# Kernel optimization log

Hardware: AMD Instinct MI355X
Metric: run time of the kernel (lower is better)

The kernel has to match this reference:

```python
import jax, jax.numpy as jnp
import numpy as np

NUM_ENTITIES = 100000
NUM_RELATIONS = 200          # 2*NUM_RELATIONS typed edges after adding inverses
DE = 200                     # entity embedding dim (= conv out channels)
DR = 200                     # relation embedding dim (in channels = DE+DR)
NUM_BASES = 4
N_NODES = 50000              # unique nodes in the extracted subgraph
N_TRIPLETS = 200000
N_EDGES = 2 * N_TRIPLETS     # forward + inverse edges


def setup_inputs() -> dict:
    key = jax.random.key(0)
    ks = jax.random.split(key, 10)
    # learned parameters
    entity_embedding = jax.random.normal(ks[0], (NUM_ENTITIES, DE), dtype=jnp.float32) * 0.05
    relation_embedding = jax.random.normal(ks[1], (NUM_RELATIONS, DR), dtype=jnp.float32) * 0.05
    # basis decomposition: W_r = sum_b att[r, b] * basis[b], basis: [B, in, out]
    xav = np.sqrt(2.0 / (DE + DR + DE)).astype(np.float32)
    basis = jax.random.normal(ks[2], (NUM_BASES, DE + DR, DE), dtype=jnp.float32) * xav
    att = jax.random.normal(ks[3], (2 * NUM_RELATIONS, NUM_BASES), dtype=jnp.float32) * 0.5
    # subgraph structure (precomputed numpy preprocessing from the torch forward)
    node_id = jax.random.randint(ks[4], (N_NODES,), 0, NUM_ENTITIES)
    src = jax.random.randint(ks[5], (N_TRIPLETS,), 0, N_NODES)
    dst = jax.random.randint(ks[6], (N_TRIPLETS,), 0, N_NODES)
    rel = jax.random.randint(ks[7], (N_TRIPLETS,), 0, NUM_RELATIONS)
    # doubling: (src->dst, rel) and inverse (dst->src, rel + NUM_RELATIONS);
    # rel_index (used to gather relation embeddings) stays un-shifted.
    edge_src = jnp.concatenate([src, dst])
    edge_dst = jnp.concatenate([dst, src])
    edge_type = jnp.concatenate([rel, rel + NUM_RELATIONS])
    rel_index = jnp.concatenate([rel, rel])
    return {
        "entity_embedding": entity_embedding,
        "relation_embedding": relation_embedding,
        "basis": basis,
        "att": att,
        "node_id": node_id,
        "edge_src": edge_src,
        "edge_dst": edge_dst,
        "edge_type": edge_type,
        "rel_index": rel_index,
        "unseen_index": 0,
    }


def reference(entity_embedding, relation_embedding, basis, att,
              node_id, edge_src, edge_dst, edge_type, rel_index, unseen_index):
    n_nodes = node_id.shape[0]
    # node features for the subgraph: [N, DE]
    x = entity_embedding[node_id]
    # per-edge relation embedding: [E, DR]
    rel = relation_embedding[rel_index]
    # message input: cat(source node emb, relation emb) -> [E, DE+DR]
    xj = jnp.concatenate([x[edge_src], rel], axis=1)
    # basis-decomposed relation-typed transform without materializing [E, in, out]:
    # project onto each basis first: [E, B, DE]
    h = jnp.einsum('ei,bio->ebo', xj, basis)
    # combine with relation-specific basis coefficients: [E, DE]
    msg = jnp.einsum('eb,ebo->eo', att[edge_type], h)
    # mean aggregation per destination node (edge_norm=None, root_weight/bias off)
    agg = jax.ops.segment_sum(msg, edge_dst, num_segments=n_nodes)
    cnt = jax.ops.segment_sum(jnp.ones(msg.shape[0], msg.dtype), edge_dst,
                              num_segments=n_nodes)
    embeddings = agg / jnp.maximum(cnt, 1.0)[:, None]
    # dropout is identity in eval mode
    return embeddings[unseen_index]
```

## Files before the change

### kernel.cpp

```cpp
#include <hip/hip_runtime.h>


#define DE 200
#define IN_DIM 400
#define ICHUNK 50
#define NCHUNK 8
#define MAXJ 32
#define FBLOCKS 256
#define TOTB (NCHUNK * MAXJ)
#define PBCAP 64
#define MAXE 128

#define WS_CNT_OFF   0
#define WS_DONE_OFF  256
#define WS_ACC_OFF   320
#define WS_LIST_OFF  1024

__global__ __launch_bounds__(256)
void filter_k(const int4* __restrict__ edge_dst4,
              const int* __restrict__ edge_dst,
              const int* __restrict__ unseen,
              int n4, int n_edges,
              int* __restrict__ ws) {
    const int b = blockIdx.x;
    const int t = threadIdx.x;
    __shared__ int s_cnt;
    __shared__ int s_list[PBCAP];
    if (t == 0) s_cnt = 0;
    __syncthreads();

    const int u = unseen[0];
    for (int idx = b * blockDim.x + t; idx < n4; idx += FBLOCKS * blockDim.x) {
        const int4 v = edge_dst4[idx];
        const int  e = idx * 4;
        if (v.x == u) { int p = atomicAdd(&s_cnt, 1); if (p < PBCAP) s_list[p] = e;     }
        if (v.y == u) { int p = atomicAdd(&s_cnt, 1); if (p < PBCAP) s_list[p] = e + 1; }
        if (v.z == u) { int p = atomicAdd(&s_cnt, 1); if (p < PBCAP) s_list[p] = e + 2; }
        if (v.w == u) { int p = atomicAdd(&s_cnt, 1); if (p < PBCAP) s_list[p] = e + 3; }
    }
    if (b == 0) {
        if (t < (n_edges & 3)) {
            const int e = n4 * 4 + t;
            if (edge_dst[e] == u) { int p = atomicAdd(&s_cnt, 1); if (p < PBCAP) s_list[p] = e; }
        }
        if (t < DE) ((float*)ws)[WS_ACC_OFF + t] = 0.f;
        if (t == DE) ws[WS_DONE_OFF] = 0;
    }
    __syncthreads();
    if (t == 0) ws[WS_CNT_OFF + b] = s_cnt;
    const int cl = s_cnt < PBCAP ? s_cnt : PBCAP;
    if (t < cl) ws[WS_LIST_OFF + b * PBCAP + t] = s_list[t];
}

__global__ __launch_bounds__(256)
void compute_k(const float* __restrict__ Eemb,
               const float* __restrict__ Remb,
               const float* __restrict__ basis,
               const float* __restrict__ att,
               const int* __restrict__ node_id,
               const int* __restrict__ edge_src,
               const int* __restrict__ edge_type,
               const int* __restrict__ rel_index,
               int* __restrict__ ws,
               float* __restrict__ out) {
    const int t = threadIdx.x;
    const int chunk = blockIdx.x;
    const int jslot = blockIdx.y;
    float* acc = (float*)ws + WS_ACC_OFF;

    __shared__ int s_counts[FBLOCKS];
    __shared__ unsigned long long s_mask[FBLOCKS / 64];
    __shared__ int s_edges[MAXE];
    __shared__ int s_total, s_listed, s_last;
    __shared__ float s_xj[ICHUNK];

    const int c = ws[WS_CNT_OFF + t];
    s_counts[t] = c;
    const unsigned long long bal = __ballot(c > 0);
    if ((t & 63) == 0) s_mask[t >> 6] = bal;
    __syncthreads();
    if (t == 0) {
        int tot = 0, listed = 0;
        for (int w = 0; w < FBLOCKS / 64; ++w) {
            unsigned long long m = s_mask[w];
            while (m) {
                const int bb = w * 64 + __builtin_ctzll(m);
                m &= m - 1;
                const int cb = s_counts[bb];
                tot += cb;
                const int cl = cb < PBCAP ? cb : PBCAP;
                for (int k = 0; k < cl && listed < MAXE; ++k)
                    s_edges[listed++] = ws[WS_LIST_OFF + bb * PBCAP + k];
            }
        }
        s_total  = tot;
        s_listed = listed;
    }
    __syncthreads();

    const int cnt  = s_listed;
    const int base = chunk * ICHUNK;

    float m = 0.f;
    bool any = false;
    for (int j = jslot; j < cnt; j += MAXJ) {
        const int e   = s_edges[j];
        const int src = edge_src[e];
        const int typ = edge_type[e];
        const int ri  = rel_index[e];
        __syncthreads();
        if (t < ICHUNK) {
            const int i = base + t;
            s_xj[t] = (i < DE) ? Eemb[(size_t)node_id[src] * DE + i]
                               : Remb[(size_t)ri * DE + (i - DE)];
        }
        __syncthreads();
        if (t < DE) {
            const float a0 = att[typ * 4 + 0];
            const float a1 = att[typ * 4 + 1];
            const float a2 = att[typ * 4 + 2];
            const float a3 = att[typ * 4 + 3];
            float h0 = 0.f, h1 = 0.f, h2 = 0.f, h3 = 0.f;
            #pragma unroll 5
            for (int ii = 0; ii < ICHUNK; ++ii) {
                const float xv  = s_xj[ii];
                const int   off = (base + ii) * DE + t;
                h0 += xv * basis[off];
                h1 += xv * basis[off + 80000];
                h2 += xv * basis[off + 160000];
                h3 += xv * basis[off + 240000];
            }
            m += a0 * h0 + a1 * h1 + a2 * h2 + a3 * h3;
            any = true;
        }
    }
    if (any) atomicAdd(&acc[t], m);

    __threadfence();
    __syncthreads();
    if (t == 0) {
        const int d = atomicAdd(&ws[WS_DONE_OFF], 1);
        s_last = (d == TOTB - 1);
    }
    __syncthreads();
    if (s_last) {
        __threadfence();
        if (t < DE) {
            const float v = atomicAdd(&acc[t], 0.f);
            int cdiv = s_total;
            if (cdiv < 1) cdiv = 1;
            out[t] = v / (float)cdiv;
        }
    }
}

extern "C" void kernel_launch(void* const* d_in, const int* in_sizes, int n_in,
                              void* d_out, int out_size, void* d_ws, size_t ws_size,
                              hipStream_t stream) {
    const float* Eemb  = (const float*)d_in[0];
    const float* Remb  = (const float*)d_in[1];
    const float* basis = (const float*)d_in[2];
    const float* att   = (const float*)d_in[3];
    const int* node_id  = (const int*)d_in[4];
    const int* edge_src = (const int*)d_in[5];
    const int* edge_dst = (const int*)d_in[6];
    const int* edge_typ = (const int*)d_in[7];
    const int* rel_idx  = (const int*)d_in[8];
    const int* unseen   = (const int*)d_in[9];
    float* out = (float*)d_out;
    int*   ws  = (int*)d_ws;

    const int n_edges = in_sizes[6];
    const int n4 = n_edges / 4;

    filter_k<<<FBLOCKS, 256, 0, stream>>>((const int4*)edge_dst, edge_dst,
                                          unseen, n4, n_edges, ws);

    dim3 cgrid(NCHUNK, MAXJ);
    compute_k<<<cgrid, 256, 0, stream>>>(Eemb, Remb, basis, att, node_id,
                                         edge_src, edge_typ, rel_idx,
                                         ws, out);
}
```

Baseline: 144.7 us.

## Reassociate per-edge basis transform into att-weighted input sums, then one GEMV per output column

The compute kernel now first forms, for each basis b, the att-weighted sum of the gathered edge inputs (a 4x400 vector), then multiplies that once by the basis matrix. Previously it ran a full per-edge projection through all bases. Each of 50 blocks prefetches its slice of basis columns into registers before the edge list is ready, and reduces through shared memory. This removes the global atomic accumulation and the last-block completion counter. In exchange, every block redundantly recomputes the 1600-entry weighted sum, and only 50 blocks run.

```diff
diff --git a/kernel.cpp b/kernel.cpp
--- a/kernel.cpp
+++ b/kernel.cpp
@@ -3,18 +3,17 @@
 
 #define DE 200
 #define IN_DIM 400
-#define ICHUNK 50
-#define NCHUNK 8
-#define MAXJ 32
+#define NB 4
+#define ROWS (NB * IN_DIM)
 #define FBLOCKS 256
-#define TOTB (NCHUNK * MAXJ)
 #define PBCAP 64
 #define MAXE 128
+#define CBLOCKS 50
+#define CPB 4
+#define KITER (ROWS / 64)
 
-#define WS_CNT_OFF   0
-#define WS_DONE_OFF  256
-#define WS_ACC_OFF   320
-#define WS_LIST_OFF  1024
+#define WS_CNT_OFF  0
+#define WS_LIST_OFF 1024
 
 __global__ __launch_bounds__(256)
 void filter_k(const int4* __restrict__ edge_dst4,
@@ -38,13 +37,9 @@
         if (v.z == u) { int p = atomicAdd(&s_cnt, 1); if (p < PBCAP) s_list[p] = e + 2; }
         if (v.w == u) { int p = atomicAdd(&s_cnt, 1); if (p < PBCAP) s_list[p] = e + 3; }
     }
-    if (b == 0) {
-        if (t < (n_edges & 3)) {
-            const int e = n4 * 4 + t;
-            if (edge_dst[e] == u) { int p = atomicAdd(&s_cnt, 1); if (p < PBCAP) s_list[p] = e; }
-        }
-        if (t < DE) ((float*)ws)[WS_ACC_OFF + t] = 0.f;
-        if (t == DE) ws[WS_DONE_OFF] = 0;
+    if (b == 0 && t < (n_edges & 3)) {
+        const int e = n4 * 4 + t;
+        if (edge_dst[e] == u) { int p = atomicAdd(&s_cnt, 1); if (p < PBCAP) s_list[p] = e; }
     }
     __syncthreads();
     if (t == 0) ws[WS_CNT_OFF + b] = s_cnt;
@@ -61,22 +56,31 @@
                const int* __restrict__ edge_src,
                const int* __restrict__ edge_type,
                const int* __restrict__ rel_index,
-               int* __restrict__ ws,
+               const int* __restrict__ ws,
                float* __restrict__ out) {
-    const int t = threadIdx.x;
-    const int chunk = blockIdx.x;
-    const int jslot = blockIdx.y;
-    float* acc = (float*)ws + WS_ACC_OFF;
+    const int t  = threadIdx.x;
+    const int c  = t & 3;
+    const int rg = t >> 2;
+    const int o  = blockIdx.x * CPB + c;
 
-    __shared__ int s_counts[FBLOCKS];
+    float rv[KITER];
+    #pragma unroll
+    for (int k = 0; k < KITER; ++k)
+        rv[k] = basis[(size_t)(rg + 64 * k) * DE + o];
+
+    __shared__ int   s_counts[FBLOCKS];
     __shared__ unsigned long long s_mask[FBLOCKS / 64];
-    __shared__ int s_edges[MAXE];
-    __shared__ int s_total, s_listed, s_last;
-    __shared__ float s_xj[ICHUNK];
+    __shared__ int   s_edges[MAXE];
+    __shared__ int   s_srcrow[MAXE];
+    __shared__ int   s_ri[MAXE];
+    __shared__ float s_att[MAXE][NB];
+    __shared__ int   s_total, s_listed;
+    __shared__ float s_y[ROWS];
+    __shared__ float s_part[256];
 
-    const int c = ws[WS_CNT_OFF + t];
-    s_counts[t] = c;
-    const unsigned long long bal = __ballot(c > 0);
+    const int cv = ws[WS_CNT_OFF + t];
+    s_counts[t] = cv;
+    const unsigned long long bal = __ballot(cv > 0);
     if ((t & 63) == 0) s_mask[t >> 6] = bal;
     __syncthreads();
     if (t == 0) {
@@ -97,60 +101,52 @@
         s_listed = listed;
     }
     __syncthreads();
+    const int cnt = s_listed;
 
-    const int cnt  = s_listed;
-    const int base = chunk * ICHUNK;
-
-    float m = 0.f;
-    bool any = false;
-    for (int j = jslot; j < cnt; j += MAXJ) {
-        const int e   = s_edges[j];
-        const int src = edge_src[e];
+    if (t < cnt) {
+        const int e = s_edges[t];
+        s_srcrow[t] = node_id[edge_src[e]];
+        s_ri[t]     = rel_index[e];
         const int typ = edge_type[e];
-        const int ri  = rel_index[e];
-        __syncthreads();
-        if (t < ICHUNK) {
-            const int i = base + t;
-            s_xj[t] = (i < DE) ? Eemb[(size_t)node_id[src] * DE + i]
-                               : Remb[(size_t)ri * DE + (i - DE)];
-        }
-        __syncthreads();
-        if (t < DE) {
-            const float a0 = att[typ * 4 + 0];
-            const float a1 = att[typ * 4 + 1];
-            const float a2 = att[typ * 4 + 2];
-            const float a3 = att[typ * 4 + 3];
-            float h0 = 0.f, h1 = 0.f, h2 = 0.f, h3 = 0.f;
-            #pragma unroll 5
-            for (int ii = 0; ii < ICHUNK; ++ii) {
-                const float xv  = s_xj[ii];
-                const int   off = (base + ii) * DE + t;
-                h0 += xv * basis[off];
-                h1 += xv * basis[off + 80000];
-                h2 += xv * basis[off + 160000];
-                h3 += xv * basis[off + 240000];
-            }
-            m += a0 * h0 + a1 * h1 + a2 * h2 + a3 * h3;
-            any = true;
-        }
-    }
-    if (any) atomicAdd(&acc[t], m);
-
-    __threadfence();
-    __syncthreads();
-    if (t == 0) {
-        const int d = atomicAdd(&ws[WS_DONE_OFF], 1);
-        s_last = (d == TOTB - 1);
+        #pragma unroll
+        for (int b = 0; b < NB; ++b) s_att[t][b] = att[typ * NB + b];
     }
     __syncthreads();
-    if (s_last) {
-        __threadfence();
-        if (t < DE) {
-            const float v = atomicAdd(&acc[t], 0.f);
-            int cdiv = s_total;
-            if (cdiv < 1) cdiv = 1;
-            out[t] = v / (float)cdiv;
+
+    for (int i = t; i < IN_DIM; i += 256) {
+        float y0 = 0.f, y1 = 0.f, y2 = 0.f, y3 = 0.f;
+        for (int j = 0; j < cnt; ++j) {
+            const float xv = (i < DE)
+                ? Eemb[(size_t)s_srcrow[j] * DE + i]
+                : Remb[(size_t)s_ri[j] * DE + (i - DE)];
+            y0 += s_att[j][0] * xv;
+            y1 += s_att[j][1] * xv;
+            y2 += s_att[j][2] * xv;
+            y3 += s_att[j][3] * xv;
         }
+        s_y[0 * IN_DIM + i] = y0;
+        s_y[1 * IN_DIM + i] = y1;
+        s_y[2 * IN_DIM + i] = y2;
+        s_y[3 * IN_DIM + i] = y3;
+    }
+    __syncthreads();
+
+    float acc = 0.f;
+    #pragma unroll
+    for (int k = 0; k < KITER; ++k)
+        acc += rv[k] * s_y[rg + 64 * k];
+
+    s_part[t] = acc;
+    __syncthreads();
+    #pragma unroll
+    for (int off = 128; off >= 4; off >>= 1) {
+        if (t < off) s_part[t] += s_part[t + off];
+        __syncthreads();
+    }
+    if (t < CPB) {
+        int cd = s_total;
+        if (cd < 1) cd = 1;
+        out[blockIdx.x * CPB + t] = s_part[t] / (float)cd;
     }
 }
 
@@ -176,8 +172,7 @@
     filter_k<<<FBLOCKS, 256, 0, stream>>>((const int4*)edge_dst, edge_dst,
                                           unseen, n4, n_edges, ws);
 
-    dim3 cgrid(NCHUNK, MAXJ);
-    compute_k<<<cgrid, 256, 0, stream>>>(Eemb, Remb, basis, att, node_id,
-                                         edge_src, edge_typ, rel_idx,
-                                         ws, out);
+    compute_k<<<CBLOCKS, 256, 0, stream>>>(Eemb, Remb, basis, att, node_id,
+                                           edge_src, edge_typ, rel_idx,
+                                           ws, out);
 }
```

Result: faster. 131.9 us (median of 2 runs) (-8.8%).
